# Kernel optimization log

Hardware: AMD Instinct MI355X
Metric: run time of the kernel (lower is better)

Reference implementation:

```python
import jax, jax.numpy as jnp
import numpy as np

DIM = 1024
NUM_HEADS = 16
HEAD_DIM = DIM // NUM_HEADS


def setup_inputs() -> dict:
    key = jax.random.key(0)
    k_x, k_q, k_k, k_v, k_o = jax.random.split(key, 5)
    B, L = 2, 2048
    scale = 1.0 / np.sqrt(DIM)
    x_bld = jax.random.normal(k_x, (B, L, DIM), dtype=jnp.float32)
    # LinearGeneral kernels: (in_features, num_heads, head_dim) for q/k/v,
    # (num_heads, head_dim, out_features) for out. Init ~ lecun_normal-ish scale.
    Wq = jax.random.normal(k_q, (DIM, NUM_HEADS, HEAD_DIM), dtype=jnp.float32) * scale
    Wk = jax.random.normal(k_k, (DIM, NUM_HEADS, HEAD_DIM), dtype=jnp.float32) * scale
    Wv = jax.random.normal(k_v, (DIM, NUM_HEADS, HEAD_DIM), dtype=jnp.float32) * scale
    Wo = jax.random.normal(k_o, (NUM_HEADS, HEAD_DIM, DIM), dtype=jnp.float32) * scale
    return {"x_bld": x_bld, "Wq": Wq, "Wk": Wk, "Wv": Wv, "Wo": Wo}


def reference(x_bld, Wq, Wk, Wv, Wo) -> jnp.ndarray:
    # Projections: [B,L,D] x [D,H,hd] -> [B,L,H,hd]
    q_blhd = jnp.einsum('bld,dhk->blhk', x_bld, Wq)
    k_blhd = jnp.einsum('bld,dhk->blhk', x_bld, Wk)
    v_blhd = jnp.einsum('bld,dhk->blhk', x_bld, Wv)
    # Scores: [B,H,L,L]
    attn_bhll = jnp.einsum('bqhd,bkhd->bhqk', q_blhd, k_blhd)
    attn_bhll = attn_bhll / jnp.sqrt(jnp.asarray(HEAD_DIM, dtype=attn_bhll.dtype))
    L = x_bld.shape[1]
    qi = jnp.arange(L)[:, None]
    ki = jnp.arange(L)[None, :]
    mask_ll = ki <= qi  # causal, no window
    neg_inf = jnp.finfo(attn_bhll.dtype).min
    attn_bhll = jnp.where(mask_ll[None, None, :, :], attn_bhll, neg_inf)
    attn_bhll = jax.nn.softmax(attn_bhll, axis=-1)
    y_blhd = jnp.einsum('bhqk,bkhd->bqhd', attn_bhll, v_blhd)
    # Output projection: contract (H, hd) -> D
    return jnp.einsum('blhk,hkd->bld', y_blhd, Wo)
```

## Files before the change

### kernel.cpp

```cpp
#include <hip/hip_runtime.h>
#include <hip/hip_bf16.h>

typedef __hip_bfloat16 bf16;
typedef __attribute__((ext_vector_type(8))) short short8;
typedef __attribute__((ext_vector_type(4))) float f32x4;
typedef __attribute__((ext_vector_type(4))) unsigned int u32x4;

__device__ __forceinline__ float bfbits2f(unsigned short u) {
    return __uint_as_float(((unsigned int)u) << 16);
}
__device__ __forceinline__ unsigned short f2bfbits(float f) {
    union { float f; unsigned int u; } x;
    x.f = f;
    unsigned int r = x.u + 0x7FFFu + ((x.u >> 16) & 1u);
    return (unsigned short)(r >> 16);
}
__device__ __forceinline__ unsigned int pack_bf16x2(float lo, float hi) {
    unsigned int u0 = __float_as_uint(lo) + 0x8000u;
    unsigned int u1 = __float_as_uint(hi) + 0x8000u;
    return __builtin_amdgcn_perm(u1, u0, 0x07060302u);
}
__device__ __forceinline__ void async_copy16(const void* g, void* l) {
    __builtin_amdgcn_global_load_lds(
        (const __attribute__((address_space(1))) void*)g,
        (__attribute__((address_space(3))) void*)l, 16, 0, 0);
}
__device__ __forceinline__ bool sniff_bf16(const unsigned int* p, int lane) {
    unsigned int wd = p[lane];
    unsigned int e = (wd >> 7) & 0xFFu;
    return __popcll(__ballot(e >= 90u && e <= 150u)) > 40;
}

__global__ __launch_bounds__(256) void prep(
    const void* __restrict__ X, const void* __restrict__ W1,
    const void* __restrict__ W2, const void* __restrict__ W3,
    const void* __restrict__ W4, short* __restrict__ xb,
    short* __restrict__ O1, short* __restrict__ O2,
    short* __restrict__ O3, short* __restrict__ O4) {
    __shared__ float tbuf[32][33];
    const int bx = blockIdx.x;
    const int tid = threadIdx.x;
    const int lane = tid & 63;

    if (bx < 2048) {
        const bool isBf = sniff_bf16((const unsigned int*)X, lane);
        const int i = (bx * 256 + tid) * 8;
        if (isBf) {
            *(short8*)&xb[i] = *(const short8*)((const short*)X + i);
        } else {
            const float* xf = (const float*)X + i;
            float4 a = *(const float4*)xf;
            float4 b = *(const float4*)(xf + 4);
            short8 o;
            o[0] = (short)f2bfbits(a.x); o[1] = (short)f2bfbits(a.y);
            o[2] = (short)f2bfbits(a.z); o[3] = (short)f2bfbits(a.w);
            o[4] = (short)f2bfbits(b.x); o[5] = (short)f2bfbits(b.y);
            o[6] = (short)f2bfbits(b.z); o[7] = (short)f2bfbits(b.w);
            *(short8*)&xb[i] = o;
        }
    } else {
        const void* Ws[4] = {W1, W2, W3, W4};
        short* Os[4] = {O1, O2, O3, O4};
        const int t = bx - 2048;
        const int wsel = t >> 10;
        const int tile = t & 1023;
        const int bxt = tile & 31, byt = tile >> 5;
        const void* W = Ws[wsel];
        const bool isBf = sniff_bf16((const unsigned int*)W, lane);
        const float scale = (wsel == 0) ? 0.18033688f : 1.0f;
        short* O = Os[wsel];

        const int tx = tid & 31, ty = tid >> 5;
        const int gx = bxt * 32 + tx;
#pragma unroll
        for (int i = 0; i < 4; i++) {
            const int gy = byt * 32 + ty + i * 8;
            float v = isBf
                ? bfbits2f(((const unsigned short*)W)[(size_t)gy * 1024 + gx])
                : ((const float*)W)[(size_t)gy * 1024 + gx];
            tbuf[ty + i * 8][tx] = v * scale;
        }
        __syncthreads();
#pragma unroll
        for (int i = 0; i < 4; i++) {
            const int orow = bxt * 32 + ty + i * 8;
            const int ocol = byt * 32 + tx;
            O[(size_t)orow * 1024 + ocol] = (short)f2bfbits(tbuf[tx][ty + i * 8]);
        }
    }
}

__global__ __launch_bounds__(256) void transpose_v(const short* __restrict__ qkv,
                                                   short* __restrict__ VtG) {
    __shared__ short t[32][33];
    const int tx = threadIdx.x & 31, ty = threadIdx.x >> 5;
    const int b = blockIdx.z >> 4, h = blockIdx.z & 15;
    const int l0 = blockIdx.x * 32, d0 = blockIdx.y * 32;
#pragma unroll
    for (int i = 0; i < 4; i++) {
        const int l = l0 + ty + i * 8;
        t[ty + i * 8][tx] =
            qkv[(size_t)(b * 2048 + l) * 3072 + 2048 + h * 64 + d0 + tx];
    }
    __syncthreads();
    const int ptx = 2 * (tx & 15) + (tx >> 4);
#pragma unroll
    for (int i = 0; i < 4; i++) {
        const int d = d0 + ty + i * 8;
        VtG[((size_t)(b * 16 + h) * 64 + d) * 2048 + l0 + ptx] = t[tx][ty + i * 8];
    }
}

template <int BN>
__global__ __launch_bounds__(256) void gemm_async(const short* __restrict__ A,
                                                  const short* __restrict__ Bt,
                                                  void* __restrict__ C,
                                                  const unsigned int* __restrict__ xdet,
                                                  int M, int N, int K) {
    __shared__ short As[2][128 * 32];
    __shared__ short Bs[2][BN * 32];
    constexpr int NI = BN / 32;

    const int tid = threadIdx.x;
    const int lane = tid & 63;
    const int wv = __builtin_amdgcn_readfirstlane(tid >> 6);
    const int quad = lane >> 4, l16 = lane & 15;
    const int wr = wv >> 1, wc = wv & 1;
    const int m0 = blockIdx.y * 128, n0 = blockIdx.x * BN;

    const int gr = lane >> 2;
    const int gc = ((lane & 3) ^ ((lane >> 3) & 3)) * 8;

    const f32x4 zero = {0.f, 0.f, 0.f, 0.f};
    f32x4 acc[4][NI];
#pragma unroll
    for (int mi = 0; mi < 4; mi++)
#pragma unroll
        for (int ni = 0; ni < NI; ni++) acc[mi][ni] = zero;

    const short* aptr[2];
    const short* bptr[BN / 64];
#pragma unroll
    for (int t = 0; t < 2; t++)
        aptr[t] = A + (size_t)(m0 + t * 64 + wv * 16 + gr) * K + gc;
#pragma unroll
    for (int t = 0; t < BN / 64; t++)
        bptr[t] = Bt + (size_t)(n0 + t * 64 + wv * 16 + gr) * K + gc;

#pragma unroll
    for (int t = 0; t < 2; t++) async_copy16(aptr[t], &As[0][(t * 64 + wv * 16) * 32]);
#pragma unroll
    for (int t = 0; t < BN / 64; t++) async_copy16(bptr[t], &Bs[0][(t * 64 + wv * 16) * 32]);

    const int ss = (quad ^ ((l16 >> 1) & 3)) * 8;

    for (int k0 = 0; k0 < K; k0 += 32) {
        const int cur = (k0 >> 5) & 1;
        __syncthreads();
        if (k0 + 32 < K) {
            const int nxt = cur ^ 1;
#pragma unroll
            for (int t = 0; t < 2; t++)
                async_copy16(aptr[t] + k0 + 32, &As[nxt][(t * 64 + wv * 16) * 32]);
#pragma unroll
            for (int t = 0; t < BN / 64; t++)
                async_copy16(bptr[t] + k0 + 32, &Bs[nxt][(t * 64 + wv * 16) * 32]);
        }

        short8 af[4], bfv[NI];
#pragma unroll
        for (int mi = 0; mi < 4; mi++)
            af[mi] = *(const short8*)&As[cur][(wr * 64 + mi * 16 + l16) * 32 + ss];
#pragma unroll
        for (int ni = 0; ni < NI; ni++)
            bfv[ni] = *(const short8*)&Bs[cur][(wc * (BN / 2) + ni * 16 + l16) * 32 + ss];
#pragma unroll
        for (int mi = 0; mi < 4; mi++)
#pragma unroll
            for (int ni = 0; ni < NI; ni++)
                acc[mi][ni] = __builtin_amdgcn_mfma_f32_16x16x32_bf16(
                    af[mi], bfv[ni], acc[mi][ni], 0, 0, 0);
    }

    bool outBf = true;
    if (xdet) outBf = sniff_bf16(xdet, lane);
    if (outBf) {
        unsigned short* Cb = (unsigned short*)C;
#pragma unroll
        for (int mi = 0; mi < 4; mi++)
#pragma unroll
            for (int ni = 0; ni < NI; ni++)
#pragma unroll
                for (int r = 0; r < 4; r++) {
                    const int row = m0 + wr * 64 + mi * 16 + quad * 4 + r;
                    const int col = n0 + wc * (BN / 2) + ni * 16 + l16;
                    Cb[(size_t)row * N + col] = f2bfbits(acc[mi][ni][r]);
                }
    } else {
        float* Cf = (float*)C;
#pragma unroll
        for (int mi = 0; mi < 4; mi++)
#pragma unroll
            for (int ni = 0; ni < NI; ni++)
#pragma unroll
                for (int r = 0; r < 4; r++) {
                    const int row = m0 + wr * 64 + mi * 16 + quad * 4 + r;
                    const int col = n0 + wc * (BN / 2) + ni * 16 + l16;
                    Cf[(size_t)row * N + col] = acc[mi][ni][r];
                }
    }
}

__global__ __launch_bounds__(256) void attn_mfma9(
    const short* __restrict__ qkv, const short* __restrict__ VtG,
    short* __restrict__ Yg, short* __restrict__ Opart, float* __restrict__ ml) {
    __shared__ short Ks[2][64 * 64];
    __shared__ short Vt[2][64 * 64];
    __shared__ float scr[16][68];
    __shared__ float lred[2][64];

    const int tid = threadIdx.x;
    const int lane = tid & 63;
    const int wv = __builtin_amdgcn_readfirstlane(tid >> 6);
    const int wvq = wv >> 1, wvk = wv & 1;
    const int quad = lane >> 4, l16 = lane & 15;
    const int bh = blockIdx.x;
    const int b = bh >> 4, h = bh & 15;

    int qb, seg, S;
    const int slot = blockIdx.y;
    if (slot < 64)      { qb = 31 - (slot >> 2); seg = slot & 3; S = 4; }
    else if (slot < 80) { const int t2 = slot - 64; qb = 15 - (t2 >> 1); seg = t2 & 1; S = 2; }
    else                { qb = 87 - slot; seg = 0; S = 1; }

    const int ns = qb + 1;
    const int sb0 = seg * ns / S;
    const int sb1 = (seg + 1) * ns / S;

    const int rr = lane >> 3;
    const int scol = ((lane & 7) ^ rr) * 8;

    const short* kptr[2];
    const short* vptr[2];
    short* kdst[2];
    short* vdst[2];
#pragma unroll
    for (int i = 0; i < 2; i++) {
        const int u = wv * 2 + i;
        kptr[i] = qkv + (size_t)(b * 2048 + sb0 * 64 + u * 8 + rr) * 3072 + 1024 +
                  h * 64 + scol;
        kdst[i] = &Ks[0][(u * 8) * 64];
        vptr[i] = VtG + ((size_t)bh * 64 + u * 8 + rr) * 2048 + sb0 * 64 + scol;
        vdst[i] = &Vt[0][(u * 8) * 64];
    }
    const int bufoff = 64 * 64;
    const int buf0 = sb0 & 1;

#pragma unroll
    for (int i = 0; i < 2; i++) {
        async_copy16(kptr[i], kdst[i] + buf0 * bufoff);
        async_copy16(vptr[i], vdst[i] + buf0 * bufoff);
        kptr[i] += 64 * 3072;
        vptr[i] += 64;
    }
    short8 qf[2][2];
    {
        const short* qbase = qkv + (size_t)(b * 2048 + qb * 64 + wvq * 32 + l16) * 3072 +
                             h * 64 + quad * 8;
#pragma unroll
        for (int qt = 0; qt < 2; qt++)
#pragma unroll
            for (int hf = 0; hf < 2; hf++)
                qf[qt][hf] = *(const short8*)(qbase + qt * 16 * 3072 + hf * 32);
    }
    __syncthreads();

    const int sl = (quad ^ (l16 & 7)) * 8;

    const f32x4 minit = {-17.3123405f, -17.3123405f, -17.3123405f, -17.3123405f};
    f32x4 O[2][4];
#pragma unroll
    for (int qt = 0; qt < 2; qt++)
#pragma unroll
        for (int dt = 0; dt < 4; dt++) O[qt][dt] = {0.f, 0.f, 0.f, 0.f};
    float lp[2] = {0.f, 0.f};
    const int keyA0 = wvk * 32 + quad * 4;

    for (int sb = sb0; sb < sb1; sb++) {
        const int cur = sb & 1;
        if (sb != sb0) __syncthreads();
        if (sb + 1 < sb1) {
            const int nxt = cur ^ 1;
#pragma unroll
            for (int i = 0; i < 2; i++) {
                async_copy16(kptr[i], kdst[i] + nxt * bufoff);
                async_copy16(vptr[i], vdst[i] + nxt * bufoff);
                kptr[i] += 64 * 3072;
                vptr[i] += 64;
            }
        }
        const short* Kc = &Ks[cur][0];
        const short* Vc = &Vt[cur][0];

        short8 kf[2][2], vf[4];
#pragma unroll
        for (int kt = 0; kt < 2; kt++)
#pragma unroll
            for (int hf = 0; hf < 2; hf++)
                kf[kt][hf] = *(const short8*)
                    &Kc[(wvk * 32 + kt * 16 + l16) * 64 + (sl ^ (hf << 5))];
#pragma unroll
        for (int dt = 0; dt < 4; dt++)
            vf[dt] = *(const short8*)
                &Vc[(dt * 16 + l16) * 64 + (sl ^ (wvk << 5))];

#pragma unroll
        for (int qt = 0; qt < 2; qt++) {
            f32x4 sA = __builtin_amdgcn_mfma_f32_16x16x32_bf16(kf[0][0], qf[qt][0], minit, 0, 0, 0);
            sA = __builtin_amdgcn_mfma_f32_16x16x32_bf16(kf[0][1], qf[qt][1], sA, 0, 0, 0);
            f32x4 sB = __builtin_amdgcn_mfma_f32_16x16x32_bf16(kf[1][0], qf[qt][0], minit, 0, 0, 0);
            sB = __builtin_amdgcn_mfma_f32_16x16x32_bf16(kf[1][1], qf[qt][1], sB, 0, 0, 0);
            if (sb == qb) {
                const int qcol = wvq * 32 + qt * 16 + l16;
#pragma unroll
                for (int r = 0; r < 4; r++) {
                    if (keyA0 + r > qcol) sA[r] = -1e30f;
                    if (keyA0 + 16 + r > qcol) sB[r] = -1e30f;
                }
            }
            union { u32x4 u; short8 s; } pa;
#pragma unroll
            for (int t = 0; t < 4; t++) {
                sA[t] = __builtin_amdgcn_exp2f(sA[t]);
                sB[t] = __builtin_amdgcn_exp2f(sB[t]);
                lp[qt] += sA[t] + sB[t];
                pa.u[t] = pack_bf16x2(sA[t], sB[t]);
            }
#pragma unroll
            for (int dt = 0; dt < 4; dt++)
                O[qt][dt] = __builtin_amdgcn_mfma_f32_16x16x32_bf16(
                    pa.s, vf[dt], O[qt][dt], 0, 0, 0);
        }
    }

#pragma unroll
    for (int qt = 0; qt < 2; qt++) {
        float v = lp[qt];
        v += __shfl_xor(v, 16);
        v += __shfl_xor(v, 32);
        if (quad == 0) lred[wvk][wvq * 32 + qt * 16 + l16] = v;
    }

#pragma unroll
    for (int g = 0; g < 2; g++)
#pragma unroll
        for (int qt = 0; qt < 2; qt++) {
            __syncthreads();
            if (wvq == g && wvk == 1) {
#pragma unroll
                for (int dt = 0; dt < 4; dt++)
#pragma unroll
                    for (int r = 0; r < 4; r++)
                        scr[quad * 4 + r][dt * 16 + l16] = O[qt][dt][r];
            }
            __syncthreads();
            if (wvq == g && wvk == 0) {
#pragma unroll
                for (int dt = 0; dt < 4; dt++)
#pragma unroll
                    for (int r = 0; r < 4; r++)
                        O[qt][dt][r] += scr[quad * 4 + r][dt * 16 + l16];
            }
        }

    if (wvk == 0) {
        if (S == 1) {
#pragma unroll
            for (int qt = 0; qt < 2; qt++)
#pragma unroll
                for (int r = 0; r < 4; r++) {
                    const int q = wvq * 32 + qt * 16 + quad * 4 + r;
                    const float inv = 1.f / (lred[0][q] + lred[1][q]);
#pragma unroll
                    for (int dt = 0; dt < 4; dt++)
                        Yg[(size_t)(b * 2048 + qb * 64 + q) * 1024 + h * 64 +
                           dt * 16 + l16] = (short)f2bfbits(O[qt][dt][r] * inv);
                }
        } else {
            const int qidx = qb - 8;
            const int base = ((seg * 32 + bh) * 24 + qidx) * 64;
#pragma unroll
            for (int qt = 0; qt < 2; qt++)
#pragma unroll
                for (int r = 0; r < 4; r++) {
                    const int q = wvq * 32 + qt * 16 + quad * 4 + r;
#pragma unroll
                    for (int dt = 0; dt < 4; dt++)
                        Opart[(size_t)(base + q) * 64 + dt * 16 + l16] =
                            (short)f2bfbits(O[qt][dt][r]);
                    if (l16 == 0) ml[base + q] = lred[0][q] + lred[1][q];
                }
        }
    }
}

__global__ __launch_bounds__(256) void attn_combine6(
    const short* __restrict__ Opart, const float* __restrict__ ml,
    short* __restrict__ Yg) {
    const int qb = 8 + blockIdx.x;
    const int bh = blockIdx.y;
    const int b = bh >> 4, h = bh & 15;
    const int S = (qb >= 16) ? 4 : 2;
    const int qidx = qb - 8;
    const int tid = threadIdx.x;
    const int q = tid >> 2;
    const int d0 = (tid & 3) * 16;

    float a0[8] = {}, a1[8] = {};
    float lsum = 0.f;
    for (int s = 0; s < S; s++) {
        const int idx = ((s * 32 + bh) * 24 + qidx) * 64 + q;
        lsum += ml[idx];
        const short* p = Opart + (size_t)idx * 64 + d0;
        short8 x0 = *(const short8*)p;
        short8 x1 = *(const short8*)(p + 8);
#pragma unroll
        for (int t = 0; t < 8; t++) {
            a0[t] += bfbits2f((unsigned short)x0[t]);
            a1[t] += bfbits2f((unsigned short)x1[t]);
        }
    }
    const float inv = 1.f / lsum;
    short8 o0, o1;
#pragma unroll
    for (int t = 0; t < 8; t++) {
        o0[t] = (short)f2bfbits(a0[t] * inv);
        o1[t] = (short)f2bfbits(a1[t] * inv);
    }
    short* yp = Yg + (size_t)(b * 2048 + qb * 64 + q) * 1024 + h * 64 + d0;
    *(short8*)yp = o0;
    *(short8*)(yp + 8) = o1;
}

extern "C" void kernel_launch(void* const* d_in, const int* in_sizes, int n_in,
                              void* d_out, int out_size, void* d_ws, size_t ws_size,
                              hipStream_t stream) {
    const int M = 2 * 2048;
    const int D = 1024;

    char* w = (char*)d_ws;
    short* xb  = (short*)w;
    short* WqT = (short*)(w + (8u << 20));
    short* WkT = WqT + (1u << 20);
    short* WvT = WkT + (1u << 20);
    short* WoT = WvT + (1u << 20);
    short* qkv = WoT + (1u << 20);
    short* VtG = qkv + (size_t)M * 3072;
    short* Opart = VtG + (size_t)2048 * 2048;
    float* mlp = (float*)(Opart + (size_t)4 * 32 * 24 * 64 * 64);
    short* y = xb;

    prep<<<6144, 256, 0, stream>>>(d_in[0], d_in[1], d_in[2], d_in[3], d_in[4],
                                   xb, WqT, WkT, WvT, WoT);

    gemm_async<128><<<dim3(3072 / 128, M / 128), 256, 0, stream>>>(
        xb, WqT, qkv, nullptr, M, 3072, D);

    transpose_v<<<dim3(64, 2, 32), 256, 0, stream>>>(qkv, VtG);

    attn_mfma9<<<dim3(32, 88), 256, 0, stream>>>(qkv, VtG, y, Opart, mlp);
    attn_combine6<<<dim3(24, 32), 256, 0, stream>>>(Opart, mlp, y);

    gemm_async<64><<<dim3(D / 64, M / 128), 256, 0, stream>>>(
        y, WoT, d_out, (const unsigned int*)d_in[0], M, D, D);
}
```

Before: 189.9 us.

## Triple-buffer K/V loads in attention with single barrier and MFMA row sums

The attention kernel moves from double to triple buffering of K/V tiles in shared memory. Each iteration now waits with a partial vmcnt and uses one barrier, so two tiles stay in flight. The softmax row sum is computed by an extra MFMA against a ones vector instead of scalar adds, and s_setprio is raised around the PV MFMAs. The cross-wave O reduction is collapsed into one write/read pass that reuses the K/V buffer as scratch, which cuts the number of barriers. The cost is more LDS per block (48KB), which may lower occupancy, plus reliance on vmcnt counting being exact.

```diff
diff --git a/kernel.cpp b/kernel.cpp
--- a/kernel.cpp
+++ b/kernel.cpp
@@ -211,12 +211,10 @@
     }
 }
 
-__global__ __launch_bounds__(256) void attn_mfma9(
+__global__ __launch_bounds__(256) void attn_mfma10(
     const short* __restrict__ qkv, const short* __restrict__ VtG,
     short* __restrict__ Yg, short* __restrict__ Opart, float* __restrict__ ml) {
-    __shared__ short Ks[2][64 * 64];
-    __shared__ short Vt[2][64 * 64];
-    __shared__ float scr[16][68];
+    __shared__ short KV[3][2][64 * 64];
     __shared__ float lred[2][64];
 
     const int tid = threadIdx.x;
@@ -249,20 +247,11 @@
         const int u = wv * 2 + i;
         kptr[i] = qkv + (size_t)(b * 2048 + sb0 * 64 + u * 8 + rr) * 3072 + 1024 +
                   h * 64 + scol;
-        kdst[i] = &Ks[0][(u * 8) * 64];
+        kdst[i] = &KV[0][0][(u * 8) * 64];
         vptr[i] = VtG + ((size_t)bh * 64 + u * 8 + rr) * 2048 + sb0 * 64 + scol;
-        vdst[i] = &Vt[0][(u * 8) * 64];
-    }
-    const int bufoff = 64 * 64;
-    const int buf0 = sb0 & 1;
-
-#pragma unroll
-    for (int i = 0; i < 2; i++) {
-        async_copy16(kptr[i], kdst[i] + buf0 * bufoff);
-        async_copy16(vptr[i], vdst[i] + buf0 * bufoff);
-        kptr[i] += 64 * 3072;
-        vptr[i] += 64;
-    }
+        vdst[i] = &KV[0][1][(u * 8) * 64];
+    }
+
     short8 qf[2][2];
     {
         const short* qbase = qkv + (size_t)(b * 2048 + qb * 64 + wvq * 32 + l16) * 3072 +
@@ -273,34 +262,46 @@
             for (int hf = 0; hf < 2; hf++)
                 qf[qt][hf] = *(const short8*)(qbase + qt * 16 * 3072 + hf * 32);
     }
-    __syncthreads();
+    asm volatile("s_waitcnt vmcnt(0)" ::: "memory");
+
+    constexpr int BUFS = 2 * 64 * 64;
+    auto STAGE = [&](int bufi) {
+#pragma unroll
+        for (int i = 0; i < 2; i++) {
+            async_copy16(kptr[i], kdst[i] + bufi * BUFS);
+            async_copy16(vptr[i], vdst[i] + bufi * BUFS);
+            kptr[i] += 64 * 3072;
+            vptr[i] += 64;
+        }
+    };
+    STAGE(0);
+    if (sb0 + 1 < sb1) STAGE(1);
 
     const int sl = (quad ^ (l16 & 7)) * 8;
 
     const f32x4 minit = {-17.3123405f, -17.3123405f, -17.3123405f, -17.3123405f};
+    const short8 vone = {(short)0x3F80, (short)0x3F80, (short)0x3F80, (short)0x3F80,
+                         (short)0x3F80, (short)0x3F80, (short)0x3F80, (short)0x3F80};
     f32x4 O[2][4];
 #pragma unroll
     for (int qt = 0; qt < 2; qt++)
 #pragma unroll
         for (int dt = 0; dt < 4; dt++) O[qt][dt] = {0.f, 0.f, 0.f, 0.f};
-    float lp[2] = {0.f, 0.f};
+    f32x4 lacc[2] = {{0.f, 0.f, 0.f, 0.f}, {0.f, 0.f, 0.f, 0.f}};
     const int keyA0 = wvk * 32 + quad * 4;
 
+    int cb = 0;
     for (int sb = sb0; sb < sb1; sb++) {
-        const int cur = sb & 1;
-        if (sb != sb0) __syncthreads();
-        if (sb + 1 < sb1) {
-            const int nxt = cur ^ 1;
-#pragma unroll
-            for (int i = 0; i < 2; i++) {
-                async_copy16(kptr[i], kdst[i] + nxt * bufoff);
-                async_copy16(vptr[i], vdst[i] + nxt * bufoff);
-                kptr[i] += 64 * 3072;
-                vptr[i] += 64;
-            }
-        }
-        const short* Kc = &Ks[cur][0];
-        const short* Vc = &Vt[cur][0];
+        if (sb + 1 < sb1) asm volatile("s_waitcnt vmcnt(4)" ::: "memory");
+        else              asm volatile("s_waitcnt vmcnt(0)" ::: "memory");
+        __builtin_amdgcn_s_barrier();
+        asm volatile("" ::: "memory");
+        if (sb + 2 < sb1) {
+            int st = cb + 2; if (st >= 3) st -= 3;
+            STAGE(st);
+        }
+        const short* Kc = &KV[cb][0][0];
+        const short* Vc = &KV[cb][1][0];
 
         short8 kf[2][2], vf[4];
 #pragma unroll
@@ -333,47 +334,51 @@
             for (int t = 0; t < 4; t++) {
                 sA[t] = __builtin_amdgcn_exp2f(sA[t]);
                 sB[t] = __builtin_amdgcn_exp2f(sB[t]);
-                lp[qt] += sA[t] + sB[t];
                 pa.u[t] = pack_bf16x2(sA[t], sB[t]);
             }
+            __builtin_amdgcn_s_setprio(1);
 #pragma unroll
             for (int dt = 0; dt < 4; dt++)
                 O[qt][dt] = __builtin_amdgcn_mfma_f32_16x16x32_bf16(
                     pa.s, vf[dt], O[qt][dt], 0, 0, 0);
-        }
-    }
-
-#pragma unroll
-    for (int qt = 0; qt < 2; qt++) {
-        float v = lp[qt];
-        v += __shfl_xor(v, 16);
-        v += __shfl_xor(v, 32);
-        if (quad == 0) lred[wvk][wvq * 32 + qt * 16 + l16] = v;
-    }
-
-#pragma unroll
-    for (int g = 0; g < 2; g++)
-#pragma unroll
-        for (int qt = 0; qt < 2; qt++) {
-            __syncthreads();
-            if (wvq == g && wvk == 1) {
-#pragma unroll
-                for (int dt = 0; dt < 4; dt++)
-#pragma unroll
-                    for (int r = 0; r < 4; r++)
-                        scr[quad * 4 + r][dt * 16 + l16] = O[qt][dt][r];
-            }
-            __syncthreads();
-            if (wvq == g && wvk == 0) {
-#pragma unroll
-                for (int dt = 0; dt < 4; dt++)
-#pragma unroll
-                    for (int r = 0; r < 4; r++)
-                        O[qt][dt][r] += scr[quad * 4 + r][dt * 16 + l16];
-            }
-        }
+            lacc[qt] = __builtin_amdgcn_mfma_f32_16x16x32_bf16(
+                pa.s, vone, lacc[qt], 0, 0, 0);
+            __builtin_amdgcn_s_setprio(0);
+        }
+        cb++; if (cb == 3) cb = 0;
+    }
+
+    if (l16 == 0) {
+#pragma unroll
+        for (int qt = 0; qt < 2; qt++)
+#pragma unroll
+            for (int r = 0; r < 4; r++)
+                lred[wvk][wvq * 32 + qt * 16 + quad * 4 + r] = lacc[qt][r];
+    }
+
+    __syncthreads();
+    float* scrf = (float*)&KV[0][0][0];
+    if (wvk == 1) {
+#pragma unroll
+        for (int qt = 0; qt < 2; qt++)
+#pragma unroll
+            for (int dt = 0; dt < 4; dt++)
+#pragma unroll
+                for (int r = 0; r < 4; r++)
+                    scrf[(wvq * 32 + qt * 16 + quad * 4 + r) * 68 + dt * 16 + l16] =
+                        O[qt][dt][r];
+    }
+    __syncthreads();
 
     if (wvk == 0) {
+#pragma unroll
+        for (int qt = 0; qt < 2; qt++)
+#pragma unroll
+            for (int dt = 0; dt < 4; dt++)
+#pragma unroll
+                for (int r = 0; r < 4; r++)
+                    O[qt][dt][r] += scrf[(wvq * 32 + qt * 16 + quad * 4 + r) * 68 +
+                                         dt * 16 + l16];
         if (S == 1) {
 #pragma unroll
             for (int qt = 0; qt < 2; qt++)
@@ -468,7 +473,7 @@
 
     transpose_v<<<dim3(64, 2, 32), 256, 0, stream>>>(qkv, VtG);
 
-    attn_mfma9<<<dim3(32, 88), 256, 0, stream>>>(qkv, VtG, y, Opart, mlp);
+    attn_mfma10<<<dim3(32, 88), 256, 0, stream>>>(qkv, VtG, y, Opart, mlp);
     attn_combine6<<<dim3(24, 32), 256, 0, stream>>>(Opart, mlp, y);
 
     gemm_async<64><<<dim3(D / 64, M / 128), 256, 0, stream>>>(
```

Result: no change. 186.6 us (-1.7%).
